# Kernel tuning notes

Measured on AMD Instinct MI355X. Metric: run time of the kernel, lower is better.

The kernel has to match this reference:

```python
import jax, jax.numpy as jnp
import numpy as np

STATE_DIM = 15


def setup_inputs() -> dict:
    key = jax.random.key(0)
    k1, k2, k3 = jax.random.split(key, 3)
    B, S = 4096, 128
    dba_params = jax.random.normal(k1, (B, S, 32), dtype=jnp.float32)
    imu_measurements = jax.random.normal(k2, (B, S, 6), dtype=jnp.float32)
    gt_state = jax.random.normal(k3, (B, S, STATE_DIM), dtype=jnp.float32)
    return {"dba_params": dba_params, "imu_measurements": imu_measurements, "gt_state": gt_state}


def reference(dba_params, imu_measurements, gt_state):
    # use_gt_init=True path: initial pose (pos + quat) taken from gt_state[:, 0, :7]
    B, S, _ = dba_params.shape
    delta = dba_params[..., :7] * 0.1          # [B, S, 7]
    init_pos = gt_state[:, 0, 0:3]              # [B, 3]
    init_q = gt_state[:, 0, 3:7]                # [B, 4]

    # Positions: pure cumulative sum of deltas (no normalization).
    pos = jnp.concatenate(
        [init_pos[:, None, :],
         init_pos[:, None, :] + jnp.cumsum(delta[:, : S - 1, 0:3], axis=1)],
        axis=1)                                 # [B, S, 3]

    # Quaternions: sequential add + renormalize each step -> lax.scan over S-1.
    def step(q, dq):
        new_q = q + dq
        new_q = new_q / jnp.linalg.norm(new_q, axis=-1, keepdims=True)
        return new_q, new_q

    dq_seq = jnp.swapaxes(delta[:, : S - 1, 3:7], 0, 1)  # [S-1, B, 4]
    _, q_steps = jax.lax.scan(step, init_q, dq_seq)       # [S-1, B, 4]
    quats = jnp.concatenate([init_q[:, None, :], jnp.swapaxes(q_steps, 0, 1)], axis=1)  # [B, S, 4]

    rest = jnp.zeros((B, S, STATE_DIM - 7), dtype=dba_params.dtype)  # channels 7:15 stay zero
    return jnp.concatenate([pos, quats, rest], axis=-1)  # [B, S, 15]
```

## Files before the change

### kernel.cpp

```cpp
#include <hip/hip_runtime.h>

#define SEQ 128
#define SD  15
#define REC 32
#define RPB 4
#define NT  (RPB * SEQ)

__global__ __launch_bounds__(NT, 8) void fused_kernel(const float* __restrict__ dba,
                                                      const float* __restrict__ gt,
                                                      float* __restrict__ out,
                                                      int B) {
    const int tid  = threadIdx.x;
    const int row  = tid >> 7;
    const int s    = tid & (SEQ - 1);
    const int lane = tid & 63;
    const int half = s >> 6;
    const int r    = blockIdx.x * RPB + row;
    const bool valid = (r < B);

    __shared__ float4 sdq  [RPB][SEQ + 1];
    __shared__ float  ginit[RPB][8];
    __shared__ float  w0tot[RPB][3];

    float d0 = 0.f, d1 = 0.f, d2 = 0.f;
    if (valid) {
        const float* rec = dba + ((size_t)r * SEQ + s) * REC;
        const float4 h0 = *reinterpret_cast<const float4*>(rec);
        const float4 h1 = *reinterpret_cast<const float4*>(rec + 4);
        sdq[row][s] = make_float4(h0.w * 0.1f, h1.x * 0.1f, h1.y * 0.1f, h1.z * 0.1f);
        d0 = h0.x * 0.1f; d1 = h0.y * 0.1f; d2 = h0.z * 0.1f;
        if (s == 0) {
            const float* g = gt + (size_t)r * SEQ * SD;
            *reinterpret_cast<float4*>(&ginit[row][0]) = *reinterpret_cast<const float4*>(g);
            *reinterpret_cast<float4*>(&ginit[row][4]) = *reinterpret_cast<const float4*>(g + 4);
        }
    }

    float ix = d0, iy = d1, iz = d2;
#pragma unroll
    for (int off = 1; off < 64; off <<= 1) {
        const float tx = __shfl_up(ix, off, 64);
        const float ty = __shfl_up(iy, off, 64);
        const float tz = __shfl_up(iz, off, 64);
        if (lane >= off) { ix += tx; iy += ty; iz += tz; }
    }
    if (half == 0 && lane == 63) {
        w0tot[row][0] = ix; w0tot[row][1] = iy; w0tot[row][2] = iz;
    }
    __syncthreads();
    if (half == 1) { ix += w0tot[row][0]; iy += w0tot[row][1]; iz += w0tot[row][2]; }

    if (valid) {
        float* o = out + ((size_t)r * SEQ + s) * SD;
        o[0] = ginit[row][0] + ix - d0;
        o[1] = ginit[row][1] + iy - d1;
        o[2] = ginit[row][2] + iz - d2;
        if (s == 0) {
            o[3] = ginit[row][3]; o[4] = ginit[row][4];
            o[5] = ginit[row][5]; o[6] = ginit[row][6];
        }
#pragma unroll
        for (int k = 7; k < SD; ++k) o[k] = 0.f;
    }

    if (tid < RPB && blockIdx.x * RPB + tid < B) {
        const float4* srow = sdq[tid];
        float* oq = out + ((size_t)(blockIdx.x * RPB + tid) * SEQ + 1) * SD + 3;
        float q0 = ginit[tid][3], q1 = ginit[tid][4],
              q2 = ginit[tid][5], q3 = ginit[tid][6];

#define QSTEP(C) do {                                                   \
            q0 += (C).x; q1 += (C).y; q2 += (C).z; q3 += (C).w;         \
            const float a_ = q0 * q0 + q1 * q1;                         \
            const float b_ = q2 * q2 + q3 * q3;                         \
            const float i_ = __builtin_amdgcn_rsqf(a_ + b_);            \
            q0 *= i_; q1 *= i_; q2 *= i_; q3 *= i_;                     \
            oq[0] = q0; oq[1] = q1; oq[2] = q2; oq[3] = q3;             \
            oq += SD;                                                   \
        } while (0)

        float4 c0 = srow[0], c1 = srow[1], c2 = srow[2], c3 = srow[3],
               c4 = srow[4], c5 = srow[5], c6 = srow[6], c7 = srow[7];
        for (int w = 0; w < 15; ++w) {
            const float4* nx = srow + (w + 1) * 8;
            const float4 n0 = nx[0], n1 = nx[1], n2 = nx[2], n3 = nx[3],
                         n4 = nx[4], n5 = nx[5], n6 = nx[6], n7 = nx[7];
            QSTEP(c0); QSTEP(c1); QSTEP(c2); QSTEP(c3);
            QSTEP(c4); QSTEP(c5); QSTEP(c6); QSTEP(c7);
            c0 = n0; c1 = n1; c2 = n2; c3 = n3;
            c4 = n4; c5 = n5; c6 = n6; c7 = n7;
        }
        QSTEP(c0); QSTEP(c1); QSTEP(c2); QSTEP(c3);
        QSTEP(c4); QSTEP(c5); QSTEP(c6);
#undef QSTEP
    }
}

extern "C" void kernel_launch(void* const* d_in, const int* in_sizes, int n_in,
                              void* d_out, int out_size, void* d_ws, size_t ws_size,
                              hipStream_t stream) {
    const float* dba = (const float*)d_in[0];
    const float* gt  = (const float*)d_in[2];
    float* out = (float*)d_out;

    const int B = in_sizes[0] / (SEQ * REC);
    const int blocks = (B + RPB - 1) / RPB;
    fused_kernel<<<blocks, NT, 0, stream>>>(dba, gt, out, B);
}
```

Before: 34.39 us.

## Stage output rows in shared memory and write back with coalesced float4 stores

The kernel now assembles each block's full output tile (positions, quaternions, zeros) in a shared-memory buffer, then after a barrier copies it to global memory with contiguous float4 stores. Previously each thread wrote its 15 scattered floats directly, and the serial quaternion thread issued strided stores, giving poorly coalesced writes. The staging buffer adds about 30KB of LDS per block, and launch bounds drop the occupancy hint from 8 to 4. The extra barrier also makes the whole block wait for the serial quaternion scan before any output is written.

```diff
diff --git a/kernel.cpp b/kernel.cpp
--- a/kernel.cpp
+++ b/kernel.cpp
@@ -5,8 +5,9 @@
 #define REC 32
 #define RPB 4
 #define NT  (RPB * SEQ)
+#define NF4 (RPB * SEQ * SD / 4)
 
-__global__ __launch_bounds__(NT, 8) void fused_kernel(const float* __restrict__ dba,
+__global__ __launch_bounds__(NT, 4) void fused_kernel(const float* __restrict__ dba,
                                                       const float* __restrict__ gt,
                                                       float* __restrict__ out,
                                                       int B) {
@@ -18,9 +19,11 @@
     const int r    = blockIdx.x * RPB + row;
     const bool valid = (r < B);
 
-    __shared__ float4 sdq  [RPB][SEQ + 1];
+    __shared__ float4 sdq[RPB][SEQ + 1];
+    __shared__ float4 pack4[NF4];
     __shared__ float  ginit[RPB][8];
     __shared__ float  w0tot[RPB][3];
+    float* pack = reinterpret_cast<float*>(pack4);
 
     float d0 = 0.f, d1 = 0.f, d2 = 0.f;
     if (valid) {
@@ -50,22 +53,22 @@
     __syncthreads();
     if (half == 1) { ix += w0tot[row][0]; iy += w0tot[row][1]; iz += w0tot[row][2]; }
 
-    if (valid) {
-        float* o = out + ((size_t)r * SEQ + s) * SD;
-        o[0] = ginit[row][0] + ix - d0;
-        o[1] = ginit[row][1] + iy - d1;
-        o[2] = ginit[row][2] + iz - d2;
+    {
+        float* rp = pack + (size_t)(row * SEQ + s) * SD;
+        rp[0] = ginit[row][0] + ix - d0;
+        rp[1] = ginit[row][1] + iy - d1;
+        rp[2] = ginit[row][2] + iz - d2;
         if (s == 0) {
-            o[3] = ginit[row][3]; o[4] = ginit[row][4];
-            o[5] = ginit[row][5]; o[6] = ginit[row][6];
+            rp[3] = ginit[row][3]; rp[4] = ginit[row][4];
+            rp[5] = ginit[row][5]; rp[6] = ginit[row][6];
         }
 #pragma unroll
-        for (int k = 7; k < SD; ++k) o[k] = 0.f;
+        for (int k = 7; k < SD; ++k) rp[k] = 0.f;
     }
 
     if (tid < RPB && blockIdx.x * RPB + tid < B) {
         const float4* srow = sdq[tid];
-        float* oq = out + ((size_t)(blockIdx.x * RPB + tid) * SEQ + 1) * SD + 3;
+        float* qp = pack + ((size_t)tid * SEQ + 1) * SD + 3;
         float q0 = ginit[tid][3], q1 = ginit[tid][4],
               q2 = ginit[tid][5], q3 = ginit[tid][6];
 
@@ -75,8 +78,8 @@
             const float b_ = q2 * q2 + q3 * q3;                         \
             const float i_ = __builtin_amdgcn_rsqf(a_ + b_);            \
             q0 *= i_; q1 *= i_; q2 *= i_; q3 *= i_;                     \
-            oq[0] = q0; oq[1] = q1; oq[2] = q2; oq[3] = q3;             \
-            oq += SD;                                                   \
+            qp[0] = q0; qp[1] = q1; qp[2] = q2; qp[3] = q3;             \
+            qp += SD;                                                   \
         } while (0)
 
         float4 c0 = srow[0], c1 = srow[1], c2 = srow[2], c3 = srow[3],
@@ -94,6 +97,14 @@
         QSTEP(c4); QSTEP(c5); QSTEP(c6);
 #undef QSTEP
     }
+    __syncthreads();
+
+    float4* ob = reinterpret_cast<float4*>(out) + (size_t)blockIdx.x * NF4;
+    const int f4PerRow = SEQ * SD / 4;
+    for (int k = tid; k < NF4; k += NT) {
+        if (blockIdx.x * RPB + k / f4PerRow < B)
+            ob[k] = pack4[k];
+    }
 }
 
 extern "C" void kernel_launch(void* const* d_in, const int* in_sizes, int n_in,
```

After: 35.76 us. +4.0%, slower.

## Map one wavefront per row and stage output in LDS for coalesced float4 stores

Applied to the files above, without the earlier changes.

Each row is now handled by a single 64-lane wavefront, with every lane covering two sequence steps. The position prefix sum and the quaternion recurrence both write into a per-wave LDS tile, which is then copied to global memory with contiguous float4 stores, replacing the old strided scalar writes. The block-wide __syncthreads and cross-half combine are gone, and s_waitcnt is used for intra-wave ordering. In exchange, LDS use per block grows to about 30KB, which may limit occupancy, and correctness depends on wave-synchronous behaviour without explicit barriers.

```diff
diff --git a/kernel.cpp b/kernel.cpp
--- a/kernel.cpp
+++ b/kernel.cpp
@@ -3,40 +3,41 @@
 #define SEQ 128
 #define SD  15
 #define REC 32
-#define RPB 4
-#define NT  (RPB * SEQ)
+#define WPB 4
+#define NT  (WPB * 64)
 
-__global__ __launch_bounds__(NT, 8) void fused_kernel(const float* __restrict__ dba,
+__global__ __launch_bounds__(NT, 4) void fused_kernel(const float* __restrict__ dba,
                                                       const float* __restrict__ gt,
                                                       float* __restrict__ out,
                                                       int B) {
     const int tid  = threadIdx.x;
-    const int row  = tid >> 7;
-    const int s    = tid & (SEQ - 1);
+    const int wave = tid >> 6;
     const int lane = tid & 63;
-    const int half = s >> 6;
-    const int r    = blockIdx.x * RPB + row;
-    const bool valid = (r < B);
+    const int r    = blockIdx.x * WPB + wave;
+    if (r >= B) return;
 
-    __shared__ float4 sdq  [RPB][SEQ + 1];
-    __shared__ float  ginit[RPB][8];
-    __shared__ float  w0tot[RPB][3];
+    __shared__ float4 sdq [WPB][SEQ];
+    __shared__ float  pack[WPB][SEQ * SD];
 
-    float d0 = 0.f, d1 = 0.f, d2 = 0.f;
-    if (valid) {
-        const float* rec = dba + ((size_t)r * SEQ + s) * REC;
-        const float4 h0 = *reinterpret_cast<const float4*>(rec);
-        const float4 h1 = *reinterpret_cast<const float4*>(rec + 4);
-        sdq[row][s] = make_float4(h0.w * 0.1f, h1.x * 0.1f, h1.y * 0.1f, h1.z * 0.1f);
-        d0 = h0.x * 0.1f; d1 = h0.y * 0.1f; d2 = h0.z * 0.1f;
-        if (s == 0) {
-            const float* g = gt + (size_t)r * SEQ * SD;
-            *reinterpret_cast<float4*>(&ginit[row][0]) = *reinterpret_cast<const float4*>(g);
-            *reinterpret_cast<float4*>(&ginit[row][4]) = *reinterpret_cast<const float4*>(g + 4);
-        }
-    }
+    const float* rec0 = dba + ((size_t)r * SEQ + 2 * lane) * REC;
+    const float4 h0a = *reinterpret_cast<const float4*>(rec0);
+    const float4 h0b = *reinterpret_cast<const float4*>(rec0 + 4);
+    const float4 h1a = *reinterpret_cast<const float4*>(rec0 + REC);
+    const float4 h1b = *reinterpret_cast<const float4*>(rec0 + REC + 4);
+    const float* g   = gt + (size_t)r * SEQ * SD;
+    const float4 gA  = *reinterpret_cast<const float4*>(g);
+    const float4 gB  = *reinterpret_cast<const float4*>(g + 4);
 
-    float ix = d0, iy = d1, iz = d2;
+    sdq[wave][2 * lane]     = make_float4(h0a.w * 0.1f, h0b.x * 0.1f,
+                                          h0b.y * 0.1f, h0b.z * 0.1f);
+    sdq[wave][2 * lane + 1] = make_float4(h1a.w * 0.1f, h1b.x * 0.1f,
+                                          h1b.y * 0.1f, h1b.z * 0.1f);
+
+    const float d0x = h0a.x * 0.1f, d0y = h0a.y * 0.1f, d0z = h0a.z * 0.1f;
+    const float d1x = h1a.x * 0.1f, d1y = h1a.y * 0.1f, d1z = h1a.z * 0.1f;
+
+    const float sx = d0x + d1x, sy = d0y + d1y, sz = d0z + d1z;
+    float ix = sx, iy = sy, iz = sz;
 #pragma unroll
     for (int off = 1; off < 64; off <<= 1) {
         const float tx = __shfl_up(ix, off, 64);
@@ -44,30 +45,29 @@
         const float tz = __shfl_up(iz, off, 64);
         if (lane >= off) { ix += tx; iy += ty; iz += tz; }
     }
-    if (half == 0 && lane == 63) {
-        w0tot[row][0] = ix; w0tot[row][1] = iy; w0tot[row][2] = iz;
-    }
-    __syncthreads();
-    if (half == 1) { ix += w0tot[row][0]; iy += w0tot[row][1]; iz += w0tot[row][2]; }
+    const float ex = ix - sx, ey = iy - sy, ez = iz - sz;
 
-    if (valid) {
-        float* o = out + ((size_t)r * SEQ + s) * SD;
-        o[0] = ginit[row][0] + ix - d0;
-        o[1] = ginit[row][1] + iy - d1;
-        o[2] = ginit[row][2] + iz - d2;
-        if (s == 0) {
-            o[3] = ginit[row][3]; o[4] = ginit[row][4];
-            o[5] = ginit[row][5]; o[6] = ginit[row][6];
+    float* pw = pack[wave];
+    {
+        float* p0 = pw + (2 * lane) * SD;
+        p0[0] = gA.x + ex; p0[1] = gA.y + ey; p0[2] = gA.z + ez;
+#pragma unroll
+        for (int k = 7; k < SD; ++k) p0[k] = 0.f;
+        float* p1 = p0 + SD;
+        p1[0] = gA.x + ex + d0x; p1[1] = gA.y + ey + d0y; p1[2] = gA.z + ez + d0z;
+#pragma unroll
+        for (int k = 7; k < SD; ++k) p1[k] = 0.f;
+        if (lane == 0) {
+            pw[3] = gA.w; pw[4] = gB.x; pw[5] = gB.y; pw[6] = gB.z;
         }
-#pragma unroll
-        for (int k = 7; k < SD; ++k) o[k] = 0.f;
     }
 
-    if (tid < RPB && blockIdx.x * RPB + tid < B) {
-        const float4* srow = sdq[tid];
-        float* oq = out + ((size_t)(blockIdx.x * RPB + tid) * SEQ + 1) * SD + 3;
-        float q0 = ginit[tid][3], q1 = ginit[tid][4],
-              q2 = ginit[tid][5], q3 = ginit[tid][6];
+    asm volatile("s_waitcnt lgkmcnt(0)" ::: "memory");
+
+    if (lane == 0) {
+        const float4* srow = sdq[wave];
+        float* qp = pw + SD + 3;
+        float q0 = gA.w, q1 = gB.x, q2 = gB.y, q3 = gB.z;
 
 #define QSTEP(C) do {                                                   \
             q0 += (C).x; q1 += (C).y; q2 += (C).z; q3 += (C).w;         \
@@ -75,8 +75,8 @@
             const float b_ = q2 * q2 + q3 * q3;                         \
             const float i_ = __builtin_amdgcn_rsqf(a_ + b_);            \
             q0 *= i_; q1 *= i_; q2 *= i_; q3 *= i_;                     \
-            oq[0] = q0; oq[1] = q1; oq[2] = q2; oq[3] = q3;             \
-            oq += SD;                                                   \
+            qp[0] = q0; qp[1] = q1; qp[2] = q2; qp[3] = q3;             \
+            qp += SD;                                                   \
         } while (0)
 
         float4 c0 = srow[0], c1 = srow[1], c2 = srow[2], c3 = srow[3],
@@ -94,6 +94,14 @@
         QSTEP(c4); QSTEP(c5); QSTEP(c6);
 #undef QSTEP
     }
+
+    asm volatile("s_waitcnt lgkmcnt(0)" ::: "memory");
+
+    float4* o4 = reinterpret_cast<float4*>(out + (size_t)r * SEQ * SD);
+    const float4* s4 = reinterpret_cast<const float4*>(pw);
+#pragma unroll
+    for (int k = lane; k < SEQ * SD / 4; k += 64)
+        o4[k] = s4[k];
 }
 
 extern "C" void kernel_launch(void* const* d_in, const int* in_sizes, int n_in,
@@ -104,6 +112,6 @@
     float* out = (float*)d_out;
 
     const int B = in_sizes[0] / (SEQ * REC);
-    const int blocks = (B + RPB - 1) / RPB;
+    const int blocks = (B + WPB - 1) / WPB;
     fused_kernel<<<blocks, NT, 0, stream>>>(dba, gt, out, B);
 }
```

Result: faster. 32.23 us (-6.3%).
